# Kernel optimization log

Measured on AMD Instinct MI355X. Metric: run time of the kernel, lower is better.

Reference implementation:

```python
import jax, jax.numpy as jnp
import numpy as np

TAU = 1.0
F_BIAS = 1.0
EPS = 1e-5


def chunk_ln(x, g, b, n):
    # layernorm applied independently over n chunks of the last dim
    B, D = x.shape
    d = D // n
    xr = x.reshape(B, n, d)
    mu = xr.mean(axis=2, keepdims=True)
    var = xr.var(axis=2, keepdims=True)
    xr = (xr - mu) / jnp.sqrt(var + EPS)
    return xr.reshape(B, D) * g + b


def setup_inputs() -> dict:
    key = jax.random.key(0)
    ks = jax.random.split(key, 16)
    B, X, H, M, K = 256, 512, 1024, 128, 64
    inp = {
        "x": jax.random.normal(ks[0], (B, X), jnp.float32),
        "c": jax.random.normal(ks[1], (B, H), jnp.float32),
        "hmem": jax.random.normal(ks[2], (B, M, H), jnp.float32),
        "u_t": jax.random.uniform(ks[3], (B, M), jnp.float32),
        "prev_read_location": jnp.zeros((B, M), jnp.float32),
        "gumbel_u": jax.random.uniform(ks[4], (B, M), jnp.float32, minval=1e-6, maxval=1.0),
        "keys": jax.random.normal(ks[5], (M, K), jnp.float32) * 0.1,
        "vec_a": jax.random.normal(ks[6], (H // 4, 1), jnp.float32) * 0.1,
        "fc_w": jax.random.normal(ks[7], (X + 2 * H + K + M, H // 4), jnp.float32) * (1.0 / np.sqrt(X + 2 * H + K + M)),
        "fc_b": jnp.zeros((H // 4,), jnp.float32),
        "W_full": jax.random.normal(ks[8], (X + 2 * H, 5 * H), jnp.float32) * (1.0 / np.sqrt(X + 2 * H)),
        "bias": jnp.zeros((5 * H,), jnp.float32),
        "W_full1": jax.random.normal(ks[9], (X + 2 * H, 2 * H), jnp.float32) * (1.0 / np.sqrt(X + 2 * H)),
        "bias1": jnp.zeros((2 * H,), jnp.float32),
        "ln1_g": jnp.ones((5 * H,), jnp.float32), "ln1_b": jnp.zeros((5 * H,), jnp.float32),
        "ln2_g": jnp.ones((H,), jnp.float32), "ln2_b": jnp.zeros((H,), jnp.float32),
        "ln3_g": jnp.ones((2 * H,), jnp.float32), "ln3_b": jnp.zeros((2 * H,), jnp.float32),
        "ln4_g": jnp.ones((M,), jnp.float32), "ln4_b": jnp.zeros((M,), jnp.float32),
    }
    return inp


def reference(x, c, hmem, u_t, prev_read_location, gumbel_u,
              keys, vec_a, fc_w, fc_b, W_full, bias, W_full1, bias1,
              ln1_g, ln1_b, ln2_g, ln2_b, ln3_g, ln3_b, ln4_g, ln4_b):
    B, X = x.shape
    H = c.shape[1]
    M = keys.shape[0]
    # --- content-addressed read head ---
    xc = jnp.concatenate([x, c], axis=1)                      # [B, X+H]
    u_norm = u_t / jnp.maximum(jnp.linalg.norm(u_t, axis=1, keepdims=True), 1e-12)
    feat = jnp.concatenate([
        jnp.broadcast_to(xc[:, None, :], (B, M, xc.shape[1])),
        jnp.broadcast_to(keys[None, :, :], (B, M, keys.shape[1])),
        hmem,
        jnp.broadcast_to(u_norm[:, None, :], (B, M, M)),
    ], axis=2)                                                # [B, M, X+2H+K+M]
    hfeat = jnp.tanh(feat @ fc_w + fc_b)                      # [B, M, H//4]
    score = jnp.einsum('bmk,k->bm', hfeat, vec_a[:, 0])       # [B, M]
    score = score - prev_read_location * 100.0
    score = chunk_ln(score, ln4_g, ln4_b, 1)
    # --- gumbel-softmax hard read (straight-through) ---
    gumbel = -jnp.log(1e-20 - jnp.log(1e-20 + gumbel_u))
    y = jax.nn.softmax((score + gumbel) * TAU, axis=1)
    ymax = jnp.max(y, axis=1, keepdims=True)
    hard = (y == ymax).astype(y.dtype)
    h_read_index = jax.lax.stop_gradient(hard - y) + y        # one-hot fwd, soft bwd
    h_entry = jnp.einsum('bm,bmh->bh', h_read_index, hmem)    # [B, H]
    # --- gated LSTM-style cell ---
    concat0 = jnp.concatenate([x, c, h_entry], axis=1)        # [B, X+2H]
    g1 = jax.nn.sigmoid(chunk_ln(concat0 @ W_full1 + bias1, ln3_g, ln3_b, 2))
    gate = jnp.concatenate([jnp.ones_like(x), g1], axis=1)
    concat0 = concat0 * gate
    z = chunk_ln(concat0 @ W_full + bias, ln1_g, ln1_b, 5)
    i, j, f, o, om = jnp.split(z, 5, axis=1)
    new_c = c * jax.nn.sigmoid(f + F_BIAS) + jax.nn.sigmoid(i) * jnp.tanh(j)
    new_c = chunk_ln(new_c, ln2_g, ln2_b, 1)
    new_h = jnp.tanh(new_c) * jax.nn.sigmoid(o)
    r = jnp.tanh(h_entry) * jax.nn.sigmoid(om)
    new_r = jnp.concatenate([new_h, r], axis=1)               # [B, 2H]
    return new_r
```

## Files before the change

kernel.cpp:

```cpp
#include <hip/hip_runtime.h>
#include <cstdint>
#include <cstddef>

typedef unsigned short u16;
typedef float floatx4 __attribute__((ext_vector_type(4)));
typedef __bf16 bf16x8 __attribute__((ext_vector_type(8)));
typedef unsigned short u16x8 __attribute__((ext_vector_type(8)));
typedef unsigned short u16x4 __attribute__((ext_vector_type(4)));

__device__ __forceinline__ u16 f2bf(float f) {
  unsigned u = __float_as_uint(f);
  unsigned r = u + 0x7FFFu + ((u >> 16) & 1u);
  return (u16)(r >> 16);
}
__device__ __forceinline__ float bf2f(u16 h) {
  return __uint_as_float(((unsigned)h) << 16);
}
__device__ __forceinline__ void gl_lds16(const void* g, void* l) {
  __builtin_amdgcn_global_load_lds(
      (const __attribute__((address_space(1))) unsigned int*)g,
      (__attribute__((address_space(3))) unsigned int*)l, 16, 0, 0);
}
__device__ __forceinline__ float wsum(float v) {
#pragma unroll
  for (int m = 32; m > 0; m >>= 1) v += __shfl_xor(v, m, 64);
  return v;
}
__device__ __forceinline__ float wmaxr(float v) {
#pragma unroll
  for (int m = 32; m > 0; m >>= 1) v = fmaxf(v, __shfl_xor(v, m, 64));
  return v;
}
template <int NW>
__device__ __forceinline__ float bsum(float v, float* sh) {
  int lane = threadIdx.x & 63, wid = threadIdx.x >> 6;
  v = wsum(v);
  __syncthreads();
  if (lane == 0) sh[wid] = v;
  __syncthreads();
  float t = 0.f;
#pragma unroll
  for (int i = 0; i < NW; ++i) t += sh[i];
  return t;
}
template <int NW>
__device__ __forceinline__ float bmaxr(float v, float* sh) {
  int lane = threadIdx.x & 63, wid = threadIdx.x >> 6;
  v = wmaxr(v);
  __syncthreads();
  if (lane == 0) sh[wid] = v;
  __syncthreads();
  float t = sh[0];
#pragma unroll
  for (int i = 1; i < NW; ++i) t = fmaxf(t, sh[i]);
  return t;
}
__device__ __forceinline__ float sigm(float x) { return 1.0f / (1.0f + expf(-x)); }

__global__ __launch_bounds__(256) void k_prep(
    const float* __restrict__ fcw, const float* __restrict__ keys,
    const float* __restrict__ ut, const float* __restrict__ fcb,
    u16* __restrict__ W3H, u16* __restrict__ W3L,
    float* __restrict__ A2, float* __restrict__ UN) {
  __shared__ float kr[64];
  __shared__ float shs[4];
  int blk = blockIdx.x, t = threadIdx.x;
  if (blk < 32) {
    int ks = blk;
    u16 hi[32], lo[32];
#pragma unroll 8
    for (int kk = 0; kk < 32; ++kk) {
      float f = fcw[(size_t)(1600 + ks * 32 + kk) * 256 + t];
      u16 h = f2bf(f);
      hi[kk] = h;
      lo[kk] = f2bf(f - bf2f(h));
    }
    u16* dh = W3H + ks * 8192 + t * 32;
    u16* dl = W3L + ks * 8192 + t * 32;
#pragma unroll
    for (int i = 0; i < 4; ++i) {
      u16x8 vh, vl;
#pragma unroll
      for (int j = 0; j < 8; ++j) { vh[j] = hi[i * 8 + j]; vl[j] = lo[i * 8 + j]; }
      *(u16x8*)&dh[i * 8] = vh;
      *(u16x8*)&dl[i * 8] = vl;
    }
  } else if (blk < 160) {
    int m = blk - 32;
    if (t < 64) kr[t] = keys[m * 64 + t];
    __syncthreads();
    float acc = fcb[t];
#pragma unroll 8
    for (int j = 0; j < 64; ++j)
      acc = fmaf(kr[j], fcw[(size_t)(1536 + j) * 256 + t], acc);
    A2[m * 256 + t] = acc;
  } else {
    int b = blk - 160;
    float v = (t < 128) ? ut[b * 128 + t] : 0.f;
    float s = bsum<4>(v * v, shs);
    float dnm = fmaxf(sqrtf(s), 1e-12f);
    if (t < 128) UN[b * 128 + t] = v / dnm;
  }
}

__global__ __launch_bounds__(256) void k_a1(
    const float* __restrict__ x, const float* __restrict__ c,
    const float* __restrict__ un, const float* __restrict__ fcw,
    float* __restrict__ A1) {
  __shared__ float sh[512];
  int kc = blockIdx.x % 26;
  int bg = blockIdx.x / 26;
  int t = threadIdx.x;
  int g0 = kc * 64;
  int row_base = (g0 < 1536) ? g0 : g0 + 1088;
#pragma unroll
  for (int p = 0; p < 2; ++p) {
    int idx = p * 256 + t;
    int bl = idx >> 6, j = idx & 63;
    int b = bg * 8 + bl;
    int g = g0 + j;
    float v;
    if (g < 512) v = x[b * 512 + g];
    else if (g < 1536) v = c[b * 1024 + (g - 512)];
    else v = un[b * 128 + (g - 1536)];
    sh[idx] = v;
  }
  __syncthreads();
  float acc[8];
#pragma unroll
  for (int i = 0; i < 8; ++i) acc[i] = 0.f;
#pragma unroll 4
  for (int j = 0; j < 64; ++j) {
    float wv = fcw[(size_t)(row_base + j) * 256 + t];
#pragma unroll
    for (int bl = 0; bl < 8; ++bl)
      acc[bl] = fmaf(sh[bl * 64 + j], wv, acc[bl]);
  }
#pragma unroll
  for (int bl = 0; bl < 8; ++bl)
    atomicAdd(&A1[(bg * 8 + bl) * 256 + t], acc[bl]);
}

__global__ __launch_bounds__(512, 2) void k2_score(
    const float* __restrict__ hmem, const u16* __restrict__ Bhp,
    const u16* __restrict__ Blp, const float* __restrict__ A1,
    const float* __restrict__ A2, const float* __restrict__ va,
    float* __restrict__ sp) {
  __shared__ __align__(16) u16 Ah[128 * 32];
  __shared__ __align__(16) u16 Al[128 * 32];
  __shared__ __align__(16) u16 Bh[256 * 32];
  __shared__ __align__(16) u16 Bl[256 * 32];
  const int b = blockIdx.x;
  const int t = threadIdx.x;
  const int lane = t & 63, w = t >> 6;
  const int q = lane >> 4, r16 = lane & 15;
  const int rh = w >> 2, cq = w & 3;

  floatx4 acc[4][4];
#pragma unroll
  for (int i = 0; i < 4; ++i)
#pragma unroll
    for (int j = 0; j < 4; ++j) acc[i][j] = (floatx4){0.f, 0.f, 0.f, 0.f};

  const int m_st = t >> 2, qh = t & 3;
  const float* aptr = hmem + ((size_t)(b * 128 + m_st)) * 1024 + qh * 8;

  float pv[8];
#pragma unroll
  for (int i = 0; i < 8; ++i) pv[i] = aptr[i];

  for (int ks = 0; ks < 32; ++ks) {
#pragma unroll
    for (int i = 0; i < 2; ++i) {
      int L = (w * 2 + i) * 1024 + lane * 16;
      gl_lds16((const char*)Bhp + (size_t)ks * 16384 + L, (char*)Bh + L);
      gl_lds16((const char*)Blp + (size_t)ks * 16384 + L, (char*)Bl + L);
    }
    u16x8 hh, ll;
#pragma unroll
    for (int i = 0; i < 8; ++i) {
      u16 h = f2bf(pv[i]);
      float hf = bf2f(h);
      hh[i] = h;
      ll[i] = f2bf(pv[i] - hf);
    }
    *(u16x8*)&Ah[m_st * 32 + qh * 8] = hh;
    *(u16x8*)&Al[m_st * 32 + qh * 8] = ll;
    __syncthreads();
    if (ks < 31) {
      const float* np = aptr + (ks + 1) * 32;
#pragma unroll
      for (int i = 0; i < 8; ++i) pv[i] = np[i];
    }
    bf16x8 ah[4], al[4];
#pragma unroll
    for (int i = 0; i < 4; ++i) {
      int row = rh * 64 + i * 16 + r16;
      ah[i] = __builtin_bit_cast(bf16x8, *(const u16x8*)&Ah[row * 32 + q * 8]);
      al[i] = __builtin_bit_cast(bf16x8, *(const u16x8*)&Al[row * 32 + q * 8]);
    }
#pragma unroll
    for (int ct = 0; ct < 4; ++ct) {
      int col = cq * 64 + ct * 16 + r16;
      bf16x8 bh = __builtin_bit_cast(bf16x8, *(const u16x8*)&Bh[col * 32 + q * 8]);
      bf16x8 bl = __builtin_bit_cast(bf16x8, *(const u16x8*)&Bl[col * 32 + q * 8]);
#pragma unroll
      for (int i = 0; i < 4; ++i) {
        acc[i][ct] = __builtin_amdgcn_mfma_f32_16x16x32_bf16(ah[i], bh, acc[i][ct], 0, 0, 0);
        acc[i][ct] = __builtin_amdgcn_mfma_f32_16x16x32_bf16(ah[i], bl, acc[i][ct], 0, 0, 0);
        acc[i][ct] = __builtin_amdgcn_mfma_f32_16x16x32_bf16(al[i], bh, acc[i][ct], 0, 0, 0);
      }
    }
    __syncthreads();
  }
  float rs[4][4];
#pragma unroll
  for (int i = 0; i < 4; ++i)
#pragma unroll
    for (int r = 0; r < 4; ++r) rs[i][r] = 0.f;
#pragma unroll
  for (int ct = 0; ct < 4; ++ct) {
    int col = cq * 64 + ct * 16 + r16;
    float a1v = A1[b * 256 + col];
    float vav = va[col];
#pragma unroll
    for (int i = 0; i < 4; ++i) {
      int row0 = rh * 64 + i * 16 + q * 4;
#pragma unroll
      for (int r = 0; r < 4; ++r) {
        float pre = acc[i][ct][r] + a1v + A2[(row0 + r) * 256 + col];
        rs[i][r] += tanhf(pre) * vav;
      }
    }
  }
#pragma unroll
  for (int mask = 1; mask <= 8; mask <<= 1)
#pragma unroll
    for (int i = 0; i < 4; ++i)
#pragma unroll
      for (int r = 0; r < 4; ++r) rs[i][r] += __shfl_xor(rs[i][r], mask, 64);
  if (r16 == 0) {
#pragma unroll
    for (int i = 0; i < 4; ++i)
#pragma unroll
      for (int r = 0; r < 4; ++r) {
        int row = rh * 64 + i * 16 + q * 4 + r;
        sp[cq * 32768 + b * 128 + row] = rs[i][r];
      }
  }
}

__global__ __launch_bounds__(128) void k3_softmax(
    const float* __restrict__ sp, const float* __restrict__ prev,
    const float* __restrict__ gu, const float* __restrict__ g4,
    const float* __restrict__ b4, float* __restrict__ wgt) {
  __shared__ float shs[2];
  int b = blockIdx.x, m = threadIdx.x;
  int bm = b * 128 + m;
  float s = sp[bm] + sp[32768 + bm] + sp[65536 + bm] + sp[98304 + bm];
  s -= prev[bm] * 100.0f;
  float mu = bsum<2>(s, shs) * (1.0f / 128.0f);
  float d = s - mu;
  float var = bsum<2>(d * d, shs) * (1.0f / 128.0f);
  float sn = d / sqrtf(var + 1e-5f) * g4[m] + b4[m];
  float gv = -logf(1e-20f - logf(1e-20f + gu[bm]));
  float z = (sn + gv) * 1.0f;
  float zm = bmaxr<2>(z, shs);
  float e = expf(z - zm);
  float Zs = bsum<2>(e, shs);
  float y = e / Zs;
  float ym = bmaxr<2>(y, shs);
  float hard = (y == ym) ? 1.0f : 0.0f;
  wgt[bm] = (hard - y) + y;
}

__global__ __launch_bounds__(256) void k4_gather(
    const float* __restrict__ wgt, const float* __restrict__ hmem,
    const float* __restrict__ x, const float* __restrict__ c,
    float* __restrict__ he, u16* __restrict__ ab1) {
  __shared__ float wsw[128];
  int b = blockIdx.x, t = threadIdx.x;
  if (t < 128) wsw[t] = wgt[b * 128 + t];
  __syncthreads();
  float4 a;
  a.x = a.y = a.z = a.w = 0.f;
  for (int mm = 0; mm < 128; ++mm) {
    float wm = wsw[mm];
    if (wm != 0.0f) {
      float4 v = ((const float4*)(hmem + ((size_t)(b * 128 + mm)) * 1024))[t];
      a.x = fmaf(wm, v.x, a.x);
      a.y = fmaf(wm, v.y, a.y);
      a.z = fmaf(wm, v.z, a.z);
      a.w = fmaf(wm, v.w, a.w);
    }
  }
  ((float4*)(he + (size_t)b * 1024))[t] = a;
  u16* row = ab1 + (size_t)b * 2560;
  if (t < 128) {
    float4 xv = ((const float4*)(x + (size_t)b * 512))[t];
    u16x4 o = {f2bf(xv.x), f2bf(xv.y), f2bf(xv.z), f2bf(xv.w)};
    *(u16x4*)&row[t * 4] = o;
  }
  {
    float4 cv = ((const float4*)(c + (size_t)b * 1024))[t];
    u16x4 o = {f2bf(cv.x), f2bf(cv.y), f2bf(cv.z), f2bf(cv.w)};
    *(u16x4*)&row[512 + t * 4] = o;
  }
  {
    u16x4 o = {f2bf(a.x), f2bf(a.y), f2bf(a.z), f2bf(a.w)};
    *(u16x4*)&row[1536 + t * 4] = o;
  }
}

__global__ __launch_bounds__(256) void gemm_cell(
    const u16* __restrict__ Abf, const float* __restrict__ W,
    float* __restrict__ Z, int N, int nblk, int nsteps) {
  __shared__ __align__(16) u16 Asm[256 * 32];
  __shared__ __align__(16) float Bf[32 * 64];
  __shared__ __align__(16) u16 Bsm[64 * 40];
  int cb = blockIdx.x % nblk;
  int kc = blockIdx.x / nblk;
  int t = threadIdx.x, lane = t & 63, w = t >> 6;
  int q = lane >> 4, r16 = lane & 15;
  floatx4 acc[4][4];
#pragma unroll
  for (int i = 0; i < 4; ++i)
#pragma unroll
    for (int j = 0; j < 4; ++j) acc[i][j] = (floatx4){0.f, 0.f, 0.f, 0.f};
  int k0 = kc * nsteps * 32;
  for (int ks = 0; ks < nsteps; ++ks) {
    int k = k0 + ks * 32;
#pragma unroll
    for (int i = 0; i < 4; ++i) {
      int L = (w * 4 + i) * 1024 + lane * 16;
      int row = L >> 6, off = L & 63;
      gl_lds16((const char*)Abf + (size_t)row * 5120 + k * 2 + off, (char*)Asm + L);
    }
#pragma unroll
    for (int i = 0; i < 2; ++i) {
      int L = (w * 2 + i) * 1024 + lane * 16;
      int kr = L >> 8, off = L & 255;
      gl_lds16((const char*)W + ((size_t)(k + kr) * N + cb * 64) * 4 + off, (char*)Bf + L);
    }
    __syncthreads();
    {
      int cc = t & 63, p = t >> 6;
      u16x8 hh;
#pragma unroll
      for (int i2 = 0; i2 < 8; ++i2) hh[i2] = f2bf(Bf[(p * 8 + i2) * 64 + cc]);
      *(u16x8*)&Bsm[cc * 40 + p * 8] = hh;
    }
    __syncthreads();
    bf16x8 af[4];
#pragma unroll
    for (int i = 0; i < 4; ++i) {
      int row = w * 64 + i * 16 + r16;
      af[i] = __builtin_bit_cast(bf16x8, *(const u16x8*)&Asm[row * 32 + q * 8]);
    }
#pragma unroll
    for (int ct = 0; ct < 4; ++ct) {
      int col = ct * 16 + r16;
      bf16x8 bb = __builtin_bit_cast(bf16x8, *(const u16x8*)&Bsm[col * 40 + q * 8]);
#pragma unroll
      for (int i = 0; i < 4; ++i)
        acc[i][ct] = __builtin_amdgcn_mfma_f32_16x16x32_bf16(af[i], bb, acc[i][ct], 0, 0, 0);
    }
    __syncthreads();
  }
#pragma unroll
  for (int ct = 0; ct < 4; ++ct)
#pragma unroll
    for (int i = 0; i < 4; ++i)
#pragma unroll
      for (int r = 0; r < 4; ++r) {
        int col = cb * 64 + ct * 16 + r16;
        int row = w * 64 + i * 16 + q * 4 + r;
        atomicAdd(&Z[(size_t)row * N + col], acc[i][ct][r]);
      }
}

__global__ __launch_bounds__(256) void k5b(
    const float* __restrict__ Z1, const float* __restrict__ bias1,
    const float* __restrict__ x, const float* __restrict__ c,
    const float* __restrict__ he, const float* __restrict__ g3,
    const float* __restrict__ b3, u16* __restrict__ ab2) {
  __shared__ float shs[4];
  int b = blockIdx.x, t = threadIdx.x;
  const float4* zp = (const float4*)(Z1 + (size_t)b * 2048);
  const float4* bp = (const float4*)bias1;
  float4 z0v = zp[t], z1v = zp[256 + t];
  float4 q0 = bp[t], q1 = bp[256 + t];
  float za[4] = {z0v.x + q0.x, z0v.y + q0.y, z0v.z + q0.z, z0v.w + q0.w};
  float zb[4] = {z1v.x + q1.x, z1v.y + q1.y, z1v.z + q1.z, z1v.w + q1.w};
  float g1a[4], g1b[4];
  {
    float s = za[0] + za[1] + za[2] + za[3];
    float mu = bsum<4>(s, shs) * (1.0f / 1024.0f);
    float ss = 0.f;
#pragma unroll
    for (int i = 0; i < 4; ++i) { float d = za[i] - mu; ss += d * d; }
    float var = bsum<4>(ss, shs) * (1.0f / 1024.0f);
    float r = sqrtf(var + 1e-5f);
    float4 gv = ((const float4*)g3)[t];
    float4 bv = ((const float4*)b3)[t];
    g1a[0] = sigm((za[0] - mu) / r * gv.x + bv.x);
    g1a[1] = sigm((za[1] - mu) / r * gv.y + bv.y);
    g1a[2] = sigm((za[2] - mu) / r * gv.z + bv.z);
    g1a[3] = sigm((za[3] - mu) / r * gv.w + bv.w);
  }
  {
    float s = zb[0] + zb[1] + zb[2] + zb[3];
    float mu = bsum<4>(s, shs) * (1.0f / 1024.0f);
    float ss = 0.f;
#pragma unroll
    for (int i = 0; i < 4; ++i) { float d = zb[i] - mu; ss += d * d; }
    float var = bsum<4>(ss, shs) * (1.0f / 1024.0f);
    float r = sqrtf(var + 1e-5f);
    float4 gv = ((const float4*)g3)[256 + t];
    float4 bv = ((const float4*)b3)[256 + t];
    g1b[0] = sigm((zb[0] - mu) / r * gv.x + bv.x);
    g1b[1] = sigm((zb[1] - mu) / r * gv.y + bv.y);
    g1b[2] = sigm((zb[2] - mu) / r * gv.z + bv.z);
    g1b[3] = sigm((zb[3] - mu) / r * gv.w + bv.w);
  }
  u16* row = ab2 + (size_t)b * 2560;
  if (t < 128) {
    float4 xv = ((const float4*)(x + (size_t)b * 512))[t];
    u16x4 o = {f2bf(xv.x), f2bf(xv.y), f2bf(xv.z), f2bf(xv.w)};
    *(u16x4*)&row[t * 4] = o;
  }
  {
    float4 cv = ((const float4*)(c + (size_t)b * 1024))[t];
    u16x4 o = {f2bf(cv.x * g1a[0]), f2bf(cv.y * g1a[1]), f2bf(cv.z * g1a[2]), f2bf(cv.w * g1a[3])};
    *(u16x4*)&row[512 + t * 4] = o;
  }
  {
    float4 hv = ((const float4*)(he + (size_t)b * 1024))[t];
    u16x4 o = {f2bf(hv.x * g1b[0]), f2bf(hv.y * g1b[1]), f2bf(hv.z * g1b[2]), f2bf(hv.w * g1b[3])};
    *(u16x4*)&row[1536 + t * 4] = o;
  }
}

__global__ __launch_bounds__(256) void k5d(
    const float* __restrict__ Z2, const float* __restrict__ bias,
    const float* __restrict__ c, const float* __restrict__ he,
    const float* __restrict__ g1, const float* __restrict__ b1,
    const float* __restrict__ g2, const float* __restrict__ b2,
    float* __restrict__ out) {
  __shared__ float shs[4];
  int b = blockIdx.x, t = threadIdx.x;
  const float4* zp = (const float4*)(Z2 + (size_t)b * 5120);
  const float4* bp = (const float4*)bias;
  float z[5][4];
#pragma unroll
  for (int ci = 0; ci < 5; ++ci) {
    float4 v = zp[ci * 256 + t];
    float4 bb = bp[ci * 256 + t];
    z[ci][0] = v.x + bb.x; z[ci][1] = v.y + bb.y;
    z[ci][2] = v.z + bb.z; z[ci][3] = v.w + bb.w;
  }
#pragma unroll
  for (int ci = 0; ci < 5; ++ci) {
    float s = z[ci][0] + z[ci][1] + z[ci][2] + z[ci][3];
    float mu = bsum<4>(s, shs) * (1.0f / 1024.0f);
    float ss = 0.f;
#pragma unroll
    for (int i = 0; i < 4; ++i) { float d = z[ci][i] - mu; ss += d * d; }
    float var = bsum<4>(ss, shs) * (1.0f / 1024.0f);
    float r = sqrtf(var + 1e-5f);
    float4 gv = ((const float4*)g1)[ci * 256 + t];
    float4 bv = ((const float4*)b1)[ci * 256 + t];
    z[ci][0] = (z[ci][0] - mu) / r * gv.x + bv.x;
    z[ci][1] = (z[ci][1] - mu) / r * gv.y + bv.y;
    z[ci][2] = (z[ci][2] - mu) / r * gv.z + bv.z;
    z[ci][3] = (z[ci][3] - mu) / r * gv.w + bv.w;
  }
  float4 cv = ((const float4*)(c + (size_t)b * 1024))[t];
  float cvv[4] = {cv.x, cv.y, cv.z, cv.w};
  float nc[4];
#pragma unroll
  for (int i = 0; i < 4; ++i)
    nc[i] = cvv[i] * sigm(z[2][i] + 1.0f) + sigm(z[0][i]) * tanhf(z[1][i]);
  float s = nc[0] + nc[1] + nc[2] + nc[3];
  float mu = bsum<4>(s, shs) * (1.0f / 1024.0f);
  float ss = 0.f;
#pragma unroll
  for (int i = 0; i < 4; ++i) { float d = nc[i] - mu; ss += d * d; }
  float var = bsum<4>(ss, shs) * (1.0f / 1024.0f);
  float r2 = sqrtf(var + 1e-5f);
  float4 g2v = ((const float4*)g2)[t];
  float4 b2v = ((const float4*)b2)[t];
  float g2a[4] = {g2v.x, g2v.y, g2v.z, g2v.w};
  float b2a[4] = {b2v.x, b2v.y, b2v.z, b2v.w};
  float4 hv = ((const float4*)(he + (size_t)b * 1024))[t];
  float hva[4] = {hv.x, hv.y, hv.z, hv.w};
  float4 o1, o2;
  float nh[4], rr[4];
#pragma unroll
  for (int i = 0; i < 4; ++i) {
    float ncn = (nc[i] - mu) / r2 * g2a[i] + b2a[i];
    nh[i] = tanhf(ncn) * sigm(z[3][i]);
    rr[i] = tanhf(hva[i]) * sigm(z[4][i]);
  }
  o1.x = nh[0]; o1.y = nh[1]; o1.z = nh[2]; o1.w = nh[3];
  o2.x = rr[0]; o2.y = rr[1]; o2.z = rr[2]; o2.w = rr[3];
  ((float4*)(out + (size_t)b * 2048))[t] = o1;
  ((float4*)(out + (size_t)b * 2048 + 1024))[t] = o2;
}

extern "C" void kernel_launch(void* const* d_in, const int* in_sizes, int n_in,
                              void* d_out, int out_size, void* d_ws, size_t ws_size,
                              hipStream_t stream) {
  const float* x = (const float*)d_in[0];
  const float* c = (const float*)d_in[1];
  const float* hmem = (const float*)d_in[2];
  const float* ut = (const float*)d_in[3];
  const float* prev = (const float*)d_in[4];
  const float* gu = (const float*)d_in[5];
  const float* keys = (const float*)d_in[6];
  const float* veca = (const float*)d_in[7];
  const float* fcw = (const float*)d_in[8];
  const float* fcb = (const float*)d_in[9];
  const float* Wf = (const float*)d_in[10];
  const float* bias = (const float*)d_in[11];
  const float* Wf1 = (const float*)d_in[12];
  const float* bias1 = (const float*)d_in[13];
  const float* ln1g = (const float*)d_in[14];
  const float* ln1b = (const float*)d_in[15];
  const float* ln2g = (const float*)d_in[16];
  const float* ln2b = (const float*)d_in[17];
  const float* ln3g = (const float*)d_in[18];
  const float* ln3b = (const float*)d_in[19];
  const float* ln4g = (const float*)d_in[20];
  const float* ln4b = (const float*)d_in[21];

  char* ws = (char*)d_ws;
  float* UN = (float*)(ws + 0);
  float* A2 = (float*)(ws + 131072);
  float* A1 = (float*)(ws + 262144);
  u16* W3H = (u16*)(ws + 524288);
  u16* W3L = (u16*)(ws + 1048576);
  float* SP = (float*)(ws + 1572864);
  float* WGT = (float*)(ws + 2097152);
  float* HE = (float*)(ws + 2228224);
  u16* AB1 = (u16*)(ws + 3276800);
  u16* AB2 = (u16*)(ws + 4587520);
  float* Z1 = (float*)(ws + 5898240);
  float* Z2 = (float*)(ws + 7995392);

  hipMemsetAsync(A1, 0, (size_t)256 * 256 * 4, stream);
  hipMemsetAsync(Z1, 0, (size_t)256 * 2048 * 4, stream);
  hipMemsetAsync(Z2, 0, (size_t)256 * 5120 * 4, stream);
  k_prep<<<416, 256, 0, stream>>>(fcw, keys, ut, fcb, W3H, W3L, A2, UN);
  k_a1<<<832, 256, 0, stream>>>(x, c, UN, fcw, A1);
  k2_score<<<256, 512, 0, stream>>>(hmem, W3H, W3L, A1, A2, veca, SP);
  k3_softmax<<<256, 128, 0, stream>>>(SP, prev, gu, ln4g, ln4b, WGT);
  k4_gather<<<256, 256, 0, stream>>>(WGT, hmem, x, c, HE, AB1);
  gemm_cell<<<32 * 8, 256, 0, stream>>>(AB1, Wf1, Z1, 2048, 32, 10);
  k5b<<<256, 256, 0, stream>>>(Z1, bias1, x, c, HE, ln3g, ln3b, AB2);
  gemm_cell<<<80 * 4, 256, 0, stream>>>(AB2, Wf, Z2, 5120, 80, 20);
  k5d<<<256, 256, 0, stream>>>(Z2, bias, c, HE, ln1g, ln1b, ln2g, ln2b, (float*)d_out);
}
```

Measured before the change: 449.6 us.

## Double-buffer score GEMM LDS tiles and XOR-swizzle A/B layouts against bank conflicts

The score kernel now double-buffers its A and B LDS tiles. The next k-slice's global-to-LDS copy and split-bf16 conversion are issued before the current slice's MFMAs, which removes one barrier per iteration. A and B tiles in the score kernel and the activation rows written by the gather/gate kernels are XOR-swizzled in 8-element slots so MFMA fragment reads avoid LDS bank conflicts. The prep kernel is split into more, smaller blocks that write the pre-swizzled weight layout. LDS use doubles, which may cut occupancy, and the swizzle must match exactly between producers and consumers.

```diff
diff --git a/kernel.cpp b/kernel.cpp
--- a/kernel.cpp
+++ b/kernel.cpp
@@ -65,28 +65,21 @@
   __shared__ float kr[64];
   __shared__ float shs[4];
   int blk = blockIdx.x, t = threadIdx.x;
-  if (blk < 32) {
-    int ks = blk;
-    u16 hi[32], lo[32];
-#pragma unroll 8
-    for (int kk = 0; kk < 32; ++kk) {
-      float f = fcw[(size_t)(1600 + ks * 32 + kk) * 256 + t];
+  if (blk < 128) {
+    int ks = blk >> 2, q = blk & 3;
+    int slot = q ^ ((t >> 1) & 3);
+    u16x8 vh, vl;
+#pragma unroll
+    for (int e = 0; e < 8; ++e) {
+      float f = fcw[(size_t)(1600 + ks * 32 + q * 8 + e) * 256 + t];
       u16 h = f2bf(f);
-      hi[kk] = h;
-      lo[kk] = f2bf(f - bf2f(h));
-    }
-    u16* dh = W3H + ks * 8192 + t * 32;
-    u16* dl = W3L + ks * 8192 + t * 32;
-#pragma unroll
-    for (int i = 0; i < 4; ++i) {
-      u16x8 vh, vl;
-#pragma unroll
-      for (int j = 0; j < 8; ++j) { vh[j] = hi[i * 8 + j]; vl[j] = lo[i * 8 + j]; }
-      *(u16x8*)&dh[i * 8] = vh;
-      *(u16x8*)&dl[i * 8] = vl;
-    }
-  } else if (blk < 160) {
-    int m = blk - 32;
+      vh[e] = h;
+      vl[e] = f2bf(f - bf2f(h));
+    }
+    *(u16x8*)&W3H[(size_t)ks * 8192 + t * 32 + slot * 8] = vh;
+    *(u16x8*)&W3L[(size_t)ks * 8192 + t * 32 + slot * 8] = vl;
+  } else if (blk < 256) {
+    int m = blk - 128;
     if (t < 64) kr[t] = keys[m * 64 + t];
     __syncthreads();
     float acc = fcb[t];
@@ -95,7 +88,7 @@
       acc = fmaf(kr[j], fcw[(size_t)(1536 + j) * 256 + t], acc);
     A2[m * 256 + t] = acc;
   } else {
-    int b = blk - 160;
+    int b = blk - 256;
     float v = (t < 128) ? ut[b * 128 + t] : 0.f;
     float s = bsum<4>(v * v, shs);
     float dnm = fmaxf(sqrtf(s), 1e-12f);
@@ -146,15 +139,16 @@
     const u16* __restrict__ Blp, const float* __restrict__ A1,
     const float* __restrict__ A2, const float* __restrict__ va,
     float* __restrict__ sp) {
-  __shared__ __align__(16) u16 Ah[128 * 32];
-  __shared__ __align__(16) u16 Al[128 * 32];
-  __shared__ __align__(16) u16 Bh[256 * 32];
-  __shared__ __align__(16) u16 Bl[256 * 32];
+  __shared__ __align__(16) u16 Ah[2][4096];
+  __shared__ __align__(16) u16 Al[2][4096];
+  __shared__ __align__(16) u16 Bh[2][8192];
+  __shared__ __align__(16) u16 Bl[2][8192];
   const int b = blockIdx.x;
   const int t = threadIdx.x;
   const int lane = t & 63, w = t >> 6;
   const int q = lane >> 4, r16 = lane & 15;
   const int rh = w >> 2, cq = w & 3;
+  const int slot = q ^ ((r16 >> 1) & 3);
 
   floatx4 acc[4][4];
 #pragma unroll
@@ -163,47 +157,80 @@
     for (int j = 0; j < 4; ++j) acc[i][j] = (floatx4){0.f, 0.f, 0.f, 0.f};
 
   const int m_st = t >> 2, qh = t & 3;
+  const int wslot = qh ^ ((m_st >> 1) & 3);
+  const int aw_idx = m_st * 32 + wslot * 8;
   const float* aptr = hmem + ((size_t)(b * 128 + m_st)) * 1024 + qh * 8;
 
+  int aoff[4], boff[4];
+#pragma unroll
+  for (int i = 0; i < 4; ++i) {
+    int row = rh * 64 + i * 16 + r16;
+    aoff[i] = row * 32 + slot * 8;
+  }
+#pragma unroll
+  for (int ct = 0; ct < 4; ++ct) {
+    int col = cq * 64 + ct * 16 + r16;
+    boff[ct] = col * 32 + slot * 8;
+  }
+
+#pragma unroll
+  for (int i = 0; i < 2; ++i) {
+    int L = (w * 2 + i) * 1024 + lane * 16;
+    gl_lds16((const char*)Bhp + L, (char*)&Bh[0][0] + L);
+    gl_lds16((const char*)Blp + L, (char*)&Bl[0][0] + L);
+  }
   float pv[8];
 #pragma unroll
   for (int i = 0; i < 8; ++i) pv[i] = aptr[i];
-
-  for (int ks = 0; ks < 32; ++ks) {
-#pragma unroll
-    for (int i = 0; i < 2; ++i) {
-      int L = (w * 2 + i) * 1024 + lane * 16;
-      gl_lds16((const char*)Bhp + (size_t)ks * 16384 + L, (char*)Bh + L);
-      gl_lds16((const char*)Blp + (size_t)ks * 16384 + L, (char*)Bl + L);
-    }
+  {
     u16x8 hh, ll;
 #pragma unroll
     for (int i = 0; i < 8; ++i) {
       u16 h = f2bf(pv[i]);
-      float hf = bf2f(h);
       hh[i] = h;
-      ll[i] = f2bf(pv[i] - hf);
-    }
-    *(u16x8*)&Ah[m_st * 32 + qh * 8] = hh;
-    *(u16x8*)&Al[m_st * 32 + qh * 8] = ll;
+      ll[i] = f2bf(pv[i] - bf2f(h));
+    }
+    *(u16x8*)&Ah[0][aw_idx] = hh;
+    *(u16x8*)&Al[0][aw_idx] = ll;
+  }
+#pragma unroll
+  for (int i = 0; i < 8; ++i) pv[i] = aptr[32 + i];
+
+  for (int ks = 0; ks < 32; ++ks) {
+    const int cur = ks & 1, nxt = cur ^ 1;
     __syncthreads();
     if (ks < 31) {
-      const float* np = aptr + (ks + 1) * 32;
-#pragma unroll
-      for (int i = 0; i < 8; ++i) pv[i] = np[i];
+#pragma unroll
+      for (int i = 0; i < 2; ++i) {
+        int L = (w * 2 + i) * 1024 + lane * 16;
+        gl_lds16((const char*)Bhp + (size_t)(ks + 1) * 16384 + L, (char*)&Bh[nxt][0] + L);
+        gl_lds16((const char*)Blp + (size_t)(ks + 1) * 16384 + L, (char*)&Bl[nxt][0] + L);
+      }
+      u16x8 hh, ll;
+#pragma unroll
+      for (int i = 0; i < 8; ++i) {
+        u16 h = f2bf(pv[i]);
+        hh[i] = h;
+        ll[i] = f2bf(pv[i] - bf2f(h));
+      }
+      *(u16x8*)&Ah[nxt][aw_idx] = hh;
+      *(u16x8*)&Al[nxt][aw_idx] = ll;
+      if (ks < 30) {
+        const float* np = aptr + (ks + 2) * 32;
+#pragma unroll
+        for (int i = 0; i < 8; ++i) pv[i] = np[i];
+      }
     }
     bf16x8 ah[4], al[4];
 #pragma unroll
     for (int i = 0; i < 4; ++i) {
-      int row = rh * 64 + i * 16 + r16;
-      ah[i] = __builtin_bit_cast(bf16x8, *(const u16x8*)&Ah[row * 32 + q * 8]);
-      al[i] = __builtin_bit_cast(bf16x8, *(const u16x8*)&Al[row * 32 + q * 8]);
+      ah[i] = __builtin_bit_cast(bf16x8, *(const u16x8*)&Ah[cur][aoff[i]]);
+      al[i] = __builtin_bit_cast(bf16x8, *(const u16x8*)&Al[cur][aoff[i]]);
     }
 #pragma unroll
     for (int ct = 0; ct < 4; ++ct) {
-      int col = cq * 64 + ct * 16 + r16;
-      bf16x8 bh = __builtin_bit_cast(bf16x8, *(const u16x8*)&Bh[col * 32 + q * 8]);
-      bf16x8 bl = __builtin_bit_cast(bf16x8, *(const u16x8*)&Bl[col * 32 + q * 8]);
+      bf16x8 bh = __builtin_bit_cast(bf16x8, *(const u16x8*)&Bh[cur][boff[ct]]);
+      bf16x8 bl = __builtin_bit_cast(bf16x8, *(const u16x8*)&Bl[cur][boff[ct]]);
 #pragma unroll
       for (int i = 0; i < 4; ++i) {
         acc[i][ct] = __builtin_amdgcn_mfma_f32_16x16x32_bf16(ah[i], bh, acc[i][ct], 0, 0, 0);
@@ -211,7 +238,6 @@
         acc[i][ct] = __builtin_amdgcn_mfma_f32_16x16x32_bf16(al[i], bh, acc[i][ct], 0, 0, 0);
       }
     }
-    __syncthreads();
   }
   float rs[4][4];
 #pragma unroll
@@ -295,20 +321,21 @@
     }
   }
   ((float4*)(he + (size_t)b * 1024))[t] = a;
+  const int sx = ((b >> 1) & 3) << 3;
   u16* row = ab1 + (size_t)b * 2560;
   if (t < 128) {
     float4 xv = ((const float4*)(x + (size_t)b * 512))[t];
     u16x4 o = {f2bf(xv.x), f2bf(xv.y), f2bf(xv.z), f2bf(xv.w)};
-    *(u16x4*)&row[t * 4] = o;
+    *(u16x4*)&row[(t * 4) ^ sx] = o;
   }
   {
     float4 cv = ((const float4*)(c + (size_t)b * 1024))[t];
     u16x4 o = {f2bf(cv.x), f2bf(cv.y), f2bf(cv.z), f2bf(cv.w)};
-    *(u16x4*)&row[512 + t * 4] = o;
+    *(u16x4*)&row[(512 + t * 4) ^ sx] = o;
   }
   {
     u16x4 o = {f2bf(a.x), f2bf(a.y), f2bf(a.z), f2bf(a.w)};
-    *(u16x4*)&row[1536 + t * 4] = o;
+    *(u16x4*)&row[(1536 + t * 4) ^ sx] = o;
   }
 }
 
@@ -322,6 +349,7 @@
   int kc = blockIdx.x / nblk;
   int t = threadIdx.x, lane = t & 63, w = t >> 6;
   int q = lane >> 4, r16 = lane & 15;
+  const int axor = ((r16 >> 1) & 3) << 3;
   floatx4 acc[4][4];
 #pragma unroll
   for (int i = 0; i < 4; ++i)
@@ -355,7 +383,7 @@
 #pragma unroll
     for (int i = 0; i < 4; ++i) {
       int row = w * 64 + i * 16 + r16;
-      af[i] = __builtin_bit_cast(bf16x8, *(const u16x8*)&Asm[row * 32 + q * 8]);
+      af[i] = __builtin_bit_cast(bf16x8, *(const u16x8*)&Asm[(row * 32 + q * 8) ^ axor]);
     }
 #pragma unroll
     for (int ct = 0; ct < 4; ++ct) {
@@ -423,21 +451,22 @@
     g1b[2] = sigm((zb[2] - mu) / r * gv.z + bv.z);
     g1b[3] = sigm((zb[3] - mu) / r * gv.w + bv.w);
   }
+  const int sx = ((b >> 1) & 3) << 3;
   u16* row = ab2 + (size_t)b * 2560;
   if (t < 128) {
     float4 xv = ((const float4*)(x + (size_t)b * 512))[t];
     u16x4 o = {f2bf(xv.x), f2bf(xv.y), f2bf(xv.z), f2bf(xv.w)};
-    *(u16x4*)&row[t * 4] = o;
+    *(u16x4*)&row[(t * 4) ^ sx] = o;
   }
   {
     float4 cv = ((const float4*)(c + (size_t)b * 1024))[t];
     u16x4 o = {f2bf(cv.x * g1a[0]), f2bf(cv.y * g1a[1]), f2bf(cv.z * g1a[2]), f2bf(cv.w * g1a[3])};
-    *(u16x4*)&row[512 + t * 4] = o;
+    *(u16x4*)&row[(512 + t * 4) ^ sx] = o;
   }
   {
     float4 hv = ((const float4*)(he + (size_t)b * 1024))[t];
     u16x4 o = {f2bf(hv.x * g1b[0]), f2bf(hv.y * g1b[1]), f2bf(hv.z * g1b[2]), f2bf(hv.w * g1b[3])};
-    *(u16x4*)&row[1536 + t * 4] = o;
+    *(u16x4*)&row[(1536 + t * 4) ^ sx] = o;
   }
 }
 
@@ -551,7 +580,7 @@
   hipMemsetAsync(A1, 0, (size_t)256 * 256 * 4, stream);
   hipMemsetAsync(Z1, 0, (size_t)256 * 2048 * 4, stream);
   hipMemsetAsync(Z2, 0, (size_t)256 * 5120 * 4, stream);
-  k_prep<<<416, 256, 0, stream>>>(fcw, keys, ut, fcb, W3H, W3L, A2, UN);
+  k_prep<<<512, 256, 0, stream>>>(fcw, keys, ut, fcb, W3H, W3L, A2, UN);
   k_a1<<<832, 256, 0, stream>>>(x, c, UN, fcw, A1);
   k2_score<<<256, 512, 0, stream>>>(hmem, W3H, W3L, A1, A2, veca, SP);
   k3_softmax<<<256, 128, 0, stream>>>(SP, prev, gu, ln4g, ln4b, WGT);
```

New measurement: 441.4 us. About the same (-1.8%).
